# Performance work log

Measured on AMD Instinct MI355X. Metric: run time of the kernel, lower is better.

The kernel has to match this reference:

```python
import jax, jax.numpy as jnp
import numpy as np

D_MODEL = 2048
N_HEADS = 32
N_KV = 8
N_REP = N_HEADS // N_KV  # 4
HEAD_DIM = D_MODEL // N_HEADS  # 64
ROPE_BASE = 10000.0
B, T = 2, 2048


def rope_tables(seq_len, head_dim):
    inv_freq = 1.0 / (ROPE_BASE ** (jnp.arange(0, head_dim, 2, dtype=jnp.float32) / head_dim))
    t = jnp.arange(seq_len, dtype=jnp.float32)
    freqs = jnp.outer(t, inv_freq)            # [T, hd/2]
    emb = jnp.concatenate([freqs, freqs], -1)  # [T, hd]
    return jnp.cos(emb), jnp.sin(emb)


def rotate_half(x):
    x1, x2 = jnp.split(x, 2, axis=-1)
    return jnp.concatenate([-x2, x1], axis=-1)


def setup_inputs() -> dict:
    key = jax.random.key(0)
    ks = jax.random.split(key, 5)
    s = D_MODEL ** -0.5
    return {
        "x": jax.random.normal(ks[0], (B, T, D_MODEL), jnp.float32),
        "Wq": jax.random.normal(ks[1], (D_MODEL, D_MODEL), jnp.float32) * s,
        "Wk": jax.random.normal(ks[2], (D_MODEL, N_KV * HEAD_DIM), jnp.float32) * s,
        "Wv": jax.random.normal(ks[3], (D_MODEL, N_KV * HEAD_DIM), jnp.float32) * s,
        "Wo": jax.random.normal(ks[4], (D_MODEL, D_MODEL), jnp.float32) * s,
    }


def reference(x, Wq, Wk, Wv, Wo):
    Bx, Tx, C = x.shape
    # QKV projections -> [B, H, T, hd]
    q = (x @ Wq).reshape(Bx, Tx, N_HEADS, HEAD_DIM).transpose(0, 2, 1, 3)
    k = (x @ Wk).reshape(Bx, Tx, N_KV, HEAD_DIM).transpose(0, 2, 1, 3)
    v = (x @ Wv).reshape(Bx, Tx, N_KV, HEAD_DIM).transpose(0, 2, 1, 3)
    # RoPE (offset=0, no cache -> prefill path)
    cos, sin = rope_tables(Tx, HEAD_DIM)  # [T, hd]
    cos = cos[None, None]
    sin = sin[None, None]
    q = q * cos + rotate_half(q) * sin
    k = k * cos + rotate_half(k) * sin
    # Grouped causal attention without materializing expanded KV:
    # q grouped as [B, n_kv, n_rep, T, hd] shares each kv head across n_rep q heads.
    scale = HEAD_DIM ** -0.5
    qg = q.reshape(Bx, N_KV, N_REP, Tx, HEAD_DIM)
    scores = jnp.einsum('bgrtd,bgsd->bgrts', qg, k) * scale  # [B, g, r, T, S]
    causal = jnp.tril(jnp.ones((Tx, Tx), dtype=bool))
    scores = jnp.where(causal, scores, jnp.float32(-jnp.inf))
    attn = jax.nn.softmax(scores, axis=-1)
    out = jnp.einsum('bgrts,bgsd->bgrtd', attn, v)  # [B, g, r, T, hd]
    out = out.reshape(Bx, N_HEADS, Tx, HEAD_DIM).transpose(0, 2, 1, 3).reshape(Bx, Tx, C)
    return out @ Wo, k, v
```

## Files before the change

kernel.cpp:

```cpp
#include <hip/hip_runtime.h>
#include <hip/hip_bf16.h>
#include <cstdint>

typedef uint16_t u16;
typedef __attribute__((ext_vector_type(8))) __bf16 bf16x8;
typedef __attribute__((ext_vector_type(4))) float f32x4;
typedef __attribute__((ext_vector_type(16))) float f32x16;
typedef __attribute__((ext_vector_type(8))) unsigned short u16x8;

#define GLD_LDS(SRC, DST) \
  __builtin_amdgcn_global_load_lds((const __attribute__((address_space(1))) void*)(SRC), \
                                   (__attribute__((address_space(3))) void*)(DST), 16, 0, 0)

#define PSWAP(d, s) asm volatile("v_permlane32_swap_b32 %0, %1" : "+v"(d), "+v"(s))

__device__ __forceinline__ u16 f2bf(float f) {
  uint32_t u = __float_as_uint(f);
  u += 0x7fffu + ((u >> 16) & 1u);
  return (u16)(u >> 16);
}

__device__ __forceinline__ float bf2f(u16 u) {
  return __uint_as_float(((uint32_t)u) << 16);
}

__device__ __forceinline__ uint32_t pk2(float a, float b) {
  union { __bf16 h[2]; uint32_t u; } x;
  x.h[0] = (__bf16)a; x.h[1] = (__bf16)b;
  return x.u;
}

__device__ __forceinline__ float fexp2(float x) {
#if __has_builtin(__builtin_amdgcn_exp2f)
  return __builtin_amdgcn_exp2f(x);
#else
  return exp2f(x);
#endif
}

__global__ __launch_bounds__(256) void prep_all(const float* __restrict__ x, u16* __restrict__ Xb,
    const float* __restrict__ Wq, const float* __restrict__ Wk, const float* __restrict__ Wv,
    u16* __restrict__ Wcat, float* __restrict__ cosT, float* __restrict__ sinT) {
  int bid = blockIdx.x, tid = threadIdx.x;
  if (bid < 2048) {
    int base = bid * 1024 + tid;
    #pragma unroll
    for (int k = 0; k < 4; ++k) {
      int i = base + k * 256;
      float4 v = reinterpret_cast<const float4*>(x)[i];
      ushort4 o;
      o.x = f2bf(v.x); o.y = f2bf(v.y); o.z = f2bf(v.z); o.w = f2bf(v.w);
      reinterpret_cast<ushort4*>(Xb)[i] = o;
    }
    return;
  }
  if (bid >= 8192) {
    int b2 = bid - 8192;
    int t = b2 * 8 + (tid >> 5), i = tid & 31;
    float invf = powf(10000.0f, -(float)i * (1.0f / 32.0f));
    float ang = (float)t * invf;
    cosT[t * 32 + i] = cosf(ang);
    sinT[t * 32 + i] = sinf(ang);
    return;
  }
  __shared__ float tile[32][33];
  const float* W; u16* Wt; int N, bx, by;
  if (bid < 6144)      { int b2 = bid - 2048; W = Wq; Wt = Wcat;               N = 2048; bx = b2 & 63; by = b2 >> 6; }
  else if (bid < 7168) { int b2 = bid - 6144; W = Wk; Wt = Wcat + 2048 * 2048; N = 512;  bx = b2 & 15; by = b2 >> 4; }
  else                 { int b2 = bid - 7168; W = Wv; Wt = Wcat + 2560 * 2048; N = 512;  bx = b2 & 15; by = b2 >> 4; }
  int n0 = bx * 32, k0 = by * 32;
  int tx = tid & 31, ty = tid >> 5;
  #pragma unroll
  for (int i = ty; i < 32; i += 8)
    tile[i][tx] = W[(size_t)(k0 + i) * N + n0 + tx];
  __syncthreads();
  #pragma unroll
  for (int i = ty; i < 32; i += 8)
    Wt[(size_t)(n0 + i) * 2048 + k0 + tx] = f2bf(tile[tx][i]);
}

__global__ __launch_bounds__(512, 2) void gemm_qkv_wot(const u16* __restrict__ A,
    const u16* __restrict__ Bt, const float* __restrict__ Wo,
    u16* __restrict__ Cq, u16* __restrict__ WoT) {
  __shared__ alignas(16) u16 Asm[2][2][256][32];
  __shared__ alignas(16) u16 Bsm[2][2][256][32];

  const int bid = blockIdx.x;
  const int tid = threadIdx.x;

  if (bid >= 192) {
    float (*tile)[65] = (float(*)[65])&Asm[0][0][0][0];
    int b2 = bid - 192;
    int r = tid >> 3, c0 = (tid & 7) * 8;
    for (int it = 0; it < 16; ++it) {
      int tI = b2 + (it << 6);
      int k0 = (tI >> 5) * 64;
      int n0 = (tI & 31) * 64;
      if (it) __syncthreads();
      float4 v0 = *reinterpret_cast<const float4*>(&Wo[(size_t)(k0 + r) * 2048 + n0 + c0]);
      float4 v1 = *reinterpret_cast<const float4*>(&Wo[(size_t)(k0 + r) * 2048 + n0 + c0 + 4]);
      tile[r][c0 + 0] = v0.x; tile[r][c0 + 1] = v0.y; tile[r][c0 + 2] = v0.z; tile[r][c0 + 3] = v0.w;
      tile[r][c0 + 4] = v1.x; tile[r][c0 + 5] = v1.y; tile[r][c0 + 6] = v1.z; tile[r][c0 + 7] = v1.w;
      __syncthreads();
      u16x8 o;
      #pragma unroll
      for (int j = 0; j < 8; ++j) o[j] = f2bf(tile[c0 + j][r]);
      *reinterpret_cast<u16x8*>(&WoT[(size_t)(n0 + r) * 2048 + k0 + c0]) = o;
    }
    return;
  }

  const int K = 2048, N = 3072;
  const int l = tid & 63;
  const int w = tid >> 6;
  const int wm = w >> 2, wn = w & 3;
  const int l15 = l & 15, l4 = l >> 4;
  const int m0 = (bid / 12) * 256, n0 = (bid % 12) * 256;
  const int NT = K >> 6;

  f32x4 acc[8][4] = {};

  const int srow = tid >> 2;
  const int sg   = (tid & 3) ^ ((srow >> 1) & 3);
  const u16* Ag = A + (size_t)(m0 + srow) * K + sg * 8;
  const u16* Bg = Bt + (size_t)(n0 + srow) * K + sg * 8;
  const size_t rsk = (size_t)128 * K;
  char* AsD = (char*)&Asm[0][0][0][0] + tid * 16;
  char* BsD = (char*)&Bsm[0][0][0][0] + tid * 16;

#define STAGE_A(BUF, KH, KT) do { \
    GLD_LDS(Ag + (KT) + (KH) * 32,       AsD + ((BUF) * 2 + (KH)) * 16384); \
    GLD_LDS(Ag + (KT) + (KH) * 32 + rsk, AsD + ((BUF) * 2 + (KH)) * 16384 + 8192); \
  } while (0)
#define STAGE_B(BUF, KH, KT) do { \
    GLD_LDS(Bg + (KT) + (KH) * 32,       BsD + ((BUF) * 2 + (KH)) * 16384); \
    GLD_LDS(Bg + (KT) + (KH) * 32 + rsk, BsD + ((BUF) * 2 + (KH)) * 16384 + 8192); \
  } while (0)

  STAGE_A(0, 0, 0);  STAGE_B(0, 0, 0);
  STAGE_A(0, 1, 0);  STAGE_B(0, 1, 0);
  STAGE_A(1, 0, 64); STAGE_B(1, 0, 64);

  const int swz = (l15 >> 1) & 3;

  for (int t = 0; t < NT; ++t) {
    const int c = t & 1;
    const int ktn  = (t + 1) << 6;
    const int ktn2 = (t + 2) << 6;
    bf16x8 bfv[4], af[4];

    if (t < NT - 1) { asm volatile("s_waitcnt vmcnt(8)" ::: "memory"); }
    else            { asm volatile("s_waitcnt vmcnt(4)" ::: "memory"); }
    asm volatile("s_barrier" ::: "memory");
    #pragma unroll
    for (int mf = 0; mf < 4; ++mf)
      af[mf] = *(const bf16x8*)&Asm[c][0][wm * 128 + mf * 16 + l15][(l4 ^ swz) * 8];
    #pragma unroll
    for (int nf = 0; nf < 4; ++nf)
      bfv[nf] = *(const bf16x8*)&Bsm[c][0][wn * 64 + nf * 16 + l15][(l4 ^ swz) * 8];
    if (t + 1 < NT) STAGE_A(c ^ 1, 1, ktn);
    __builtin_amdgcn_s_setprio(1);
    #pragma unroll
    for (int mf = 0; mf < 4; ++mf)
      #pragma unroll
      for (int nf = 0; nf < 4; ++nf)
        acc[mf][nf] = __builtin_amdgcn_mfma_f32_16x16x32_bf16(af[mf], bfv[nf], acc[mf][nf], 0, 0, 0);
    __builtin_amdgcn_s_setprio(0);
    asm volatile("s_barrier" ::: "memory");

    #pragma unroll
    for (int mf = 0; mf < 4; ++mf)
      af[mf] = *(const bf16x8*)&Asm[c][0][wm * 128 + 64 + mf * 16 + l15][(l4 ^ swz) * 8];
    if (t + 1 < NT) STAGE_B(c ^ 1, 1, ktn);
    __builtin_amdgcn_s_setprio(1);
    #pragma unroll
    for (int mf = 0; mf < 4; ++mf)
      #pragma unroll
      for (int nf = 0; nf < 4; ++nf)
        acc[4 + mf][nf] = __builtin_amdgcn_mfma_f32_16x16x32_bf16(af[mf], bfv[nf], acc[4 + mf][nf], 0, 0, 0);
    __builtin_amdgcn_s_setprio(0);
    asm volatile("s_barrier" ::: "memory");

    if (t < NT - 1) { asm volatile("s_waitcnt vmcnt(8)" ::: "memory"); }
    else            { asm volatile("s_waitcnt vmcnt(0)" ::: "memory"); }
    asm volatile("s_barrier" ::: "memory");
    #pragma unroll
    for (int mf = 0; mf < 4; ++mf)
      af[mf] = *(const bf16x8*)&Asm[c][1][wm * 128 + mf * 16 + l15][(l4 ^ swz) * 8];
    #pragma unroll
    for (int nf = 0; nf < 4; ++nf)
      bfv[nf] = *(const bf16x8*)&Bsm[c][1][wn * 64 + nf * 16 + l15][(l4 ^ swz) * 8];
    if (t + 2 < NT) STAGE_A(c, 0, ktn2);
    __builtin_amdgcn_s_setprio(1);
    #pragma unroll
    for (int mf = 0; mf < 4; ++mf)
      #pragma unroll
      for (int nf = 0; nf < 4; ++nf)
        acc[mf][nf] = __builtin_amdgcn_mfma_f32_16x16x32_bf16(af[mf], bfv[nf], acc[mf][nf], 0, 0, 0);
    __builtin_amdgcn_s_setprio(0);
    asm volatile("s_barrier" ::: "memory");

    #pragma unroll
    for (int mf = 0; mf < 4; ++mf)
      af[mf] = *(const bf16x8*)&Asm[c][1][wm * 128 + 64 + mf * 16 + l15][(l4 ^ swz) * 8];
    if (t + 2 < NT) STAGE_B(c, 0, ktn2);
    __builtin_amdgcn_s_setprio(1);
    #pragma unroll
    for (int mf = 0; mf < 4; ++mf)
      #pragma unroll
      for (int nf = 0; nf < 4; ++nf)
        acc[4 + mf][nf] = __builtin_amdgcn_mfma_f32_16x16x32_bf16(af[mf], bfv[nf], acc[4 + mf][nf], 0, 0, 0);
    __builtin_amdgcn_s_setprio(0);
    asm volatile("s_barrier" ::: "memory");
  }
#undef STAGE_A
#undef STAGE_B

  #pragma unroll
  for (int mi = 0; mi < 8; ++mi)
    #pragma unroll
    for (int nf = 0; nf < 4; ++nf)
      #pragma unroll
      for (int r = 0; r < 4; ++r) {
        int row = m0 + wm * 128 + mi * 16 + l4 * 4 + r;
        int col = n0 + wn * 64 + nf * 16 + l15;
        Cq[(size_t)row * N + col] = f2bf(acc[mi][nf][r]);
      }
}

__global__ __launch_bounds__(512, 2) void gemm128(const u16* __restrict__ A,
    const u16* __restrict__ Bt, float* __restrict__ C, int M, int N, int K) {
  __shared__ alignas(16) u16 Asm[2][2][128][32];
  __shared__ alignas(16) u16 Bsm[2][2][256][32];

  const int tid = threadIdx.x;
  const int l = tid & 63;
  const int w = tid >> 6;
  const int wm = w >> 2, wn = w & 3;
  const int l15 = l & 15, l4 = l >> 4;
  const int m0 = blockIdx.y * 128, n0 = blockIdx.x * 256;
  const int NT = K >> 6;

  f32x4 acc[4][4] = {};

  const int srow = tid >> 2;
  const int sg   = (tid & 3) ^ ((srow >> 1) & 3);
  const u16* Ag = A + (size_t)(m0 + srow) * K + sg * 8;
  const u16* Bg = Bt + (size_t)(n0 + srow) * K + sg * 8;
  const size_t rsk = (size_t)128 * K;
  char* AsD = (char*)&Asm[0][0][0][0] + tid * 16;
  char* BsD = (char*)&Bsm[0][0][0][0] + tid * 16;

#define STG(BUF, KH, KT) do { \
    GLD_LDS(Ag + (KT) + (KH) * 32,       AsD + ((BUF) * 2 + (KH)) * 8192); \
    GLD_LDS(Bg + (KT) + (KH) * 32,       BsD + ((BUF) * 2 + (KH)) * 16384); \
    GLD_LDS(Bg + (KT) + (KH) * 32 + rsk, BsD + ((BUF) * 2 + (KH)) * 16384 + 8192); \
  } while (0)

  STG(0, 0, 0); STG(0, 1, 0); STG(1, 0, 64);

  const int swz = (l15 >> 1) & 3;

  for (int t = 0; t < NT; ++t) {
    const int c = t & 1;
    bf16x8 af[4], bfv[4];

    if (t < NT - 1) { asm volatile("s_waitcnt vmcnt(6)" ::: "memory"); }
    else            { asm volatile("s_waitcnt vmcnt(3)" ::: "memory"); }
    asm volatile("s_barrier" ::: "memory");
    #pragma unroll
    for (int mf = 0; mf < 4; ++mf)
      af[mf] = *(const bf16x8*)&Asm[c][0][wm * 64 + mf * 16 + l15][(l4 ^ swz) * 8];
    #pragma unroll
    for (int nf = 0; nf < 4; ++nf)
      bfv[nf] = *(const bf16x8*)&Bsm[c][0][wn * 64 + nf * 16 + l15][(l4 ^ swz) * 8];
    if (t + 1 < NT) STG(c ^ 1, 1, (t + 1) << 6);
    __builtin_amdgcn_s_setprio(1);
    #pragma unroll
    for (int mf = 0; mf < 4; ++mf)
      #pragma unroll
      for (int nf = 0; nf < 4; ++nf)
        acc[mf][nf] = __builtin_amdgcn_mfma_f32_16x16x32_bf16(af[mf], bfv[nf], acc[mf][nf], 0, 0, 0);
    __builtin_amdgcn_s_setprio(0);
    asm volatile("s_barrier" ::: "memory");

    if (t < NT - 1) { asm volatile("s_waitcnt vmcnt(6)" ::: "memory"); }
    else            { asm volatile("s_waitcnt vmcnt(0)" ::: "memory"); }
    asm volatile("s_barrier" ::: "memory");
    #pragma unroll
    for (int mf = 0; mf < 4; ++mf)
      af[mf] = *(const bf16x8*)&Asm[c][1][wm * 64 + mf * 16 + l15][(l4 ^ swz) * 8];
    #pragma unroll
    for (int nf = 0; nf < 4; ++nf)
      bfv[nf] = *(const bf16x8*)&Bsm[c][1][wn * 64 + nf * 16 + l15][(l4 ^ swz) * 8];
    if (t + 2 < NT) STG(c, 0, (t + 2) << 6);
    __builtin_amdgcn_s_setprio(1);
    #pragma unroll
    for (int mf = 0; mf < 4; ++mf)
      #pragma unroll
      for (int nf = 0; nf < 4; ++nf)
        acc[mf][nf] = __builtin_amdgcn_mfma_f32_16x16x32_bf16(af[mf], bfv[nf], acc[mf][nf], 0, 0, 0);
    __builtin_amdgcn_s_setprio(0);
    asm volatile("s_barrier" ::: "memory");
  }
#undef STG

  #pragma unroll
  for (int mf = 0; mf < 4; ++mf)
    #pragma unroll
    for (int nf = 0; nf < 4; ++nf)
      #pragma unroll
      for (int r = 0; r < 4; ++r) {
        int row = m0 + wm * 64 + mf * 16 + l4 * 4 + r;
        int col = n0 + wn * 64 + nf * 16 + l15;
        C[(size_t)row * N + col] = acc[mf][nf][r];
      }
}

__global__ __launch_bounds__(256) void rope_scatter(const u16* __restrict__ QKV,
    const float* __restrict__ cosT, const float* __restrict__ sinT,
    u16* __restrict__ Qr, u16* __restrict__ Kr,
    float* __restrict__ outK, float* __restrict__ outV) {
  const float QSCALE = 0.125f * 1.44269504088896f;
  int row = blockIdx.x;
  int b = row >> 11, t = row & 2047;
  const u16* src = QKV + (size_t)row * 3072;
  int tid = threadIdx.x;
  #pragma unroll
  for (int p = tid; p < 1024; p += 256) {
    int h = p >> 5, d = p & 31;
    float c = cosT[t * 32 + d], s = sinT[t * 32 + d];
    float q0 = bf2f(src[h * 64 + d]), q1 = bf2f(src[h * 64 + d + 32]);
    size_t base = ((size_t)(b * 32 + h) * 2048 + t) * 64 + d;
    Qr[base]      = f2bf((q0 * c - q1 * s) * QSCALE);
    Qr[base + 32] = f2bf((q1 * c + q0 * s) * QSCALE);
  }
  {
    int p = tid;
    int gk = p >> 5, d = p & 31;
    float c = cosT[t * 32 + d], s = sinT[t * 32 + d];
    float k0 = bf2f(src[2048 + gk * 64 + d]), k1 = bf2f(src[2048 + gk * 64 + d + 32]);
    float r0 = k0 * c - k1 * s, r1 = k1 * c + k0 * s;
    size_t base = ((size_t)(b * 8 + gk) * 2048 + t) * 64 + d;
    Kr[base] = f2bf(r0); Kr[base + 32] = f2bf(r1);
    outK[base] = r0; outK[base + 32] = r1;
  }
  #pragma unroll
  for (int p = tid; p < 512; p += 256) {
    int gv = p >> 6, d = p & 63;
    size_t base = ((size_t)(b * 8 + gv) * 2048 + t) * 64 + d;
    outV[base] = bf2f(src[2560 + gv * 64 + d]);
  }
}

__global__ __launch_bounds__(256) void v_transpose(const float* __restrict__ src, u16* __restrict__ dst) {
  __shared__ float tile[64][65];
  int tt = blockIdx.x, bg = blockIdx.y;
  int tid = threadIdx.x;
  const float* sp = src + (size_t)bg * 2048 * 64 + (size_t)tt * 64 * 64;
  int tl = tid >> 2, c0 = (tid & 3) * 16;
  #pragma unroll
  for (int i = 0; i < 4; ++i) {
    float4 v = *reinterpret_cast<const float4*>(sp + (size_t)tl * 64 + c0 + i * 4);
    tile[tl][c0 + i * 4 + 0] = v.x;
    tile[tl][c0 + i * 4 + 1] = v.y;
    tile[tl][c0 + i * 4 + 2] = v.z;
    tile[tl][c0 + i * 4 + 3] = v.w;
  }
  __syncthreads();
  int d = tid >> 2, j0 = (tid & 3) * 16;
  u16x8 a, c;
  #pragma unroll
  for (int j = 0; j < 8; ++j) a[j] = f2bf(tile[j0 + j][d]);
  #pragma unroll
  for (int j = 0; j < 8; ++j) c[j] = f2bf(tile[j0 + 8 + j][d]);
  u16* dp = dst + (size_t)bg * 64 * 2048 + (size_t)d * 2048 + tt * 64 + j0;
  *reinterpret_cast<u16x8*>(dp) = a;
  *reinterpret_cast<u16x8*>(dp + 8) = c;
}

__global__ __launch_bounds__(256) void attn_kernel(
    const u16* __restrict__ Qr, const u16* __restrict__ Kr,
    const u16* __restrict__ Vt, u16* __restrict__ Ao) {
  __shared__ alignas(16) u16 Ks[2][64][72];
  __shared__ alignas(16) u16 Vs[2][64][72];

  const float FIXEDM = 24.0f;

  int bid = blockIdx.x;
  int pairI = bid >> 5;
  int sub = (bid >> 4) & 1;
  int g   = (bid >> 1) & 7;
  int b   = bid & 1;
  int tid = threadIdx.x;
  int w = tid >> 6, l = tid & 63;
  int l31 = l & 31, hi = l >> 5;
  int h = g * 4 + w;

  const u16* Kh = Kr + (size_t)(b * 8 + g) * 2048 * 64;
  const u16* Vh = Vt + (size_t)(b * 8 + g) * 64 * 2048;

  union { u16x8 u; bf16x8 v; } ones;
  #pragma unroll
  for (int i = 0; i < 8; ++i) ones.u[i] = 0x3F80;

  int srow = tid >> 2, sc0 = (tid & 3) * 16;
  const u16* Kp = Kh + (size_t)srow * 64 + sc0;
  const u16* Vp = Vh + (size_t)srow * 2048 + sc0;

  for (int half = 0; half < 2; ++half) {
    const int qc  = half ? pairI : (31 - pairI);
    const int q0w = qc * 64 + sub * 32;
    const int qg  = q0w + l31;

    const u16* Qh = Qr + ((size_t)(b * 32 + h) * 2048 + q0w) * 64;
    bf16x8 qf[4];
    #pragma unroll
    for (int t = 0; t < 4; ++t)
      qf[t] = *reinterpret_cast<const bf16x8*>(Qh + (size_t)l31 * 64 + t * 16 + hi * 8);

    f32x16 o0 = {}, o1 = {}, lacc = {};

    if (half) __syncthreads();

    {
      bf16x8 k0v = *reinterpret_cast<const bf16x8*>(Kp);
      bf16x8 k1v = *reinterpret_cast<const bf16x8*>(Kp + 8);
      bf16x8 v0v = *reinterpret_cast<const bf16x8*>(Vp);
      bf16x8 v1v = *reinterpret_cast<const bf16x8*>(Vp + 8);
      *reinterpret_cast<bf16x8*>(&Ks[0][srow][sc0]) = k0v;
      *reinterpret_cast<bf16x8*>(&Ks[0][srow][sc0 + 8]) = k1v;
      *reinterpret_cast<bf16x8*>(&Vs[0][srow][sc0]) = v0v;
      *reinterpret_cast<bf16x8*>(&Vs[0][srow][sc0 + 8]) = v1v;
    }
    __syncthreads();

    for (int s = 0; s <= qc; ++s) {
      int cur = s & 1;
      bf16x8 knx0, knx1, vnx0, vnx1;
      if (s < qc) {
        knx0 = *reinterpret_cast<const bf16x8*>(Kp + (size_t)(s + 1) * 4096);
        knx1 = *reinterpret_cast<const bf16x8*>(Kp + (size_t)(s + 1) * 4096 + 8);
        vnx0 = *reinterpret_cast<const bf16x8*>(Vp + (size_t)(s + 1) * 64);
        vnx1 = *reinterpret_cast<const bf16x8*>(Vp + (size_t)(s + 1) * 64 + 8);
      }
      int nh = (s == qc && sub == 0) ? 1 : 2;

      f32x16 s0, s1;
      #pragma unroll
      for (int r = 0; r < 16; ++r) { s0[r] = -FIXEDM; s1[r] = -FIXEDM; }

      __builtin_amdgcn_s_setprio(1);
      #pragma unroll
      for (int t = 0; t < 4; ++t) {
        bf16x8 kf0 = *reinterpret_cast<const bf16x8*>(&Ks[cur][l31][t * 16 + hi * 8]);
        s0 = __builtin_amdgcn_mfma_f32_32x32x16_bf16(kf0, qf[t], s0, 0, 0, 0);
      }
      if (nh == 2) {
        #pragma unroll
        for (int t = 0; t < 4; ++t) {
          bf16x8 kf1 = *reinterpret_cast<const bf16x8*>(&Ks[cur][32 + l31][t * 16 + hi * 8]);
          s1 = __builtin_amdgcn_mfma_f32_32x32x16_bf16(kf1, qf[t], s1, 0, 0, 0);
        }
      }
      __builtin_amdgcn_s_setprio(0);

      if (s == qc) {
        #pragma unroll
        for (int r = 0; r < 16; ++r) {
          int kvg = s * 64 + (r & 3) + (r >> 2) * 8 + hi * 4;
          if (kvg > qg) s0[r] = -INFINITY;
        }
        if (nh == 2) {
          #pragma unroll
          for (int r = 0; r < 16; ++r) {
            int kvg = s * 64 + 32 + (r & 3) + (r >> 2) * 8 + hi * 4;
            if (kvg > qg) s1[r] = -INFINITY;
          }
        }
      }

      float p0[16], p1[16];
      #pragma unroll
      for (int r = 0; r < 16; ++r) p0[r] = fexp2(s0[r]);
      if (nh == 2) {
        #pragma unroll
        for (int r = 0; r < 16; ++r) p1[r] = fexp2(s1[r]);
      }

      uint32_t pkA[8], pkB[8];
      #pragma unroll
      for (int gi = 0; gi < 8; ++gi) {
        if (gi < nh * 4) {
          const float* pp = (gi < 4) ? p0 : p1;
          int base = (gi & 3) * 4;
          pkA[gi] = pk2(pp[base + 0], pp[base + 1]);
          pkB[gi] = pk2(pp[base + 2], pp[base + 3]);
        }
      }
      __builtin_amdgcn_s_setprio(1);
      #pragma unroll
      for (int kc = 0; kc < 4; ++kc) {
        if (kc < nh * 2) {
          uint32_t wd0 = pkA[kc * 2], wd2 = pkA[kc * 2 + 1];
          PSWAP(wd0, wd2);
          uint32_t wd1 = pkB[kc * 2], wd3 = pkB[kc * 2 + 1];
          PSWAP(wd1, wd3);
          union { uint32_t wd[4]; bf16x8 v; } pb;
          pb.wd[0] = wd0; pb.wd[1] = wd1; pb.wd[2] = wd2; pb.wd[3] = wd3;
          bf16x8 va0 = *reinterpret_cast<const bf16x8*>(&Vs[cur][l31][kc * 16 + hi * 8]);
          bf16x8 va1 = *reinterpret_cast<const bf16x8*>(&Vs[cur][32 + l31][kc * 16 + hi * 8]);
          o0 = __builtin_amdgcn_mfma_f32_32x32x16_bf16(va0, pb.v, o0, 0, 0, 0);
          o1 = __builtin_amdgcn_mfma_f32_32x32x16_bf16(va1, pb.v, o1, 0, 0, 0);
          lacc = __builtin_amdgcn_mfma_f32_32x32x16_bf16(ones.v, pb.v, lacc, 0, 0, 0);
        }
      }
      __builtin_amdgcn_s_setprio(0);

      if (s < qc) {
        *reinterpret_cast<bf16x8*>(&Ks[cur ^ 1][srow][sc0]) = knx0;
        *reinterpret_cast<bf16x8*>(&Ks[cur ^ 1][srow][sc0 + 8]) = knx1;
        *reinterpret_cast<bf16x8*>(&Vs[cur ^ 1][srow][sc0]) = vnx0;
        *reinterpret_cast<bf16x8*>(&Vs[cur ^ 1][srow][sc0 + 8]) = vnx1;
        __syncthreads();
      }
    }

    float inv = 1.0f / lacc[0];
    int token = b * 2048 + q0w + l31;
    u16* dst = Ao + (size_t)token * 2048 + h * 64;
    #pragma unroll
    for (int hf = 0; hf < 2; ++hf) {
      f32x16 ov = hf ? o1 : o0;
      #pragma unroll
      for (int r = 0; r < 16; r += 2) {
        int d = (r & 3) + (r >> 2) * 8 + hi * 4 + hf * 32;
        *reinterpret_cast<uint32_t*>(dst + d) = pk2(ov[r] * inv, ov[r + 1] * inv);
      }
    }
  }
}

extern "C" void kernel_launch(void* const* d_in, const int* in_sizes, int n_in,
                              void* d_out, int out_size, void* d_ws, size_t ws_size,
                              hipStream_t stream) {
  const float* x  = (const float*)d_in[0];
  const float* Wq = (const float*)d_in[1];
  const float* Wk = (const float*)d_in[2];
  const float* Wv = (const float*)d_in[3];
  const float* Wo = (const float*)d_in[4];
  float* out = (float*)d_out;

  char* ws = (char*)d_ws;
  u16*   Xb    = (u16*)(ws + 0);
  u16*   Wcat  = (u16*)(ws + 16777216);
  u16*   WoT   = (u16*)(ws + 29360128);
  u16*   QKV   = (u16*)(ws + 37748736);
  u16*   AttnB = (u16*)(ws + 37748736);
  u16*   Qr    = (u16*)(ws + 88080384);
  u16*   Kr    = (u16*)(ws + 104857600);
  u16*   Vtr   = (u16*)(ws + 109051904);
  float* cosT  = (float*)(ws + 113246208);
  float* sinT  = (float*)(ws + 113508352);

  float* outK = out + 8388608;
  float* outV = out + 10485760;

  prep_all<<<8448, 256, 0, stream>>>(x, Xb, Wq, Wk, Wv, Wcat, cosT, sinT);
  gemm_qkv_wot<<<256, 512, 0, stream>>>(Xb, Wcat, Wo, QKV, WoT);
  rope_scatter<<<4096, 256, 0, stream>>>(QKV, cosT, sinT, Qr, Kr, outK, outV);
  v_transpose<<<dim3(32, 16), 256, 0, stream>>>(outV, Vtr);
  attn_kernel<<<512, 256, 0, stream>>>(Qr, Kr, Vtr, AttnB);
  gemm128<<<dim3(8, 32), 512, 0, stream>>>(AttnB, WoT, out, 4096, 2048, 2048);
}
```

Before: 202.7 us.

## Move Wo transpose into prep kernel and retile QKV GEMM to 128x384

The Wo fp32-to-bf16 transpose moves out of the QKV GEMM kernel and into the prep kernel as extra 32x32 tile blocks. The QKV GEMM is retiled from 256x256 blocks with a 2x4 warp grid to 128x384 blocks, each warp owning a 128x48 strip, launched as an 8x32 grid of 256 blocks. The aim is to spread the GEMM evenly across CUs without the transpose blocks sharing its launch, and to simplify the staging schedule. In exchange, A-fragment reuse per warp drops, and the launch bound no longer requests two blocks per CU.

Result: slower. 210.8 us (+4.0%).

```diff
diff --git a/kernel.cpp b/kernel.cpp
--- a/kernel.cpp
+++ b/kernel.cpp
@@ -40,7 +40,8 @@
 
 __global__ __launch_bounds__(256) void prep_all(const float* __restrict__ x, u16* __restrict__ Xb,
     const float* __restrict__ Wq, const float* __restrict__ Wk, const float* __restrict__ Wv,
-    u16* __restrict__ Wcat, float* __restrict__ cosT, float* __restrict__ sinT) {
+    const float* __restrict__ Wo, u16* __restrict__ Wcat, u16* __restrict__ WoT,
+    float* __restrict__ cosT, float* __restrict__ sinT) {
   int bid = blockIdx.x, tid = threadIdx.x;
   if (bid < 2048) {
     int base = bid * 1024 + tid;
@@ -54,7 +55,7 @@
     }
     return;
   }
-  if (bid >= 8192) {
+  if (bid >= 8192 && bid < 8448) {
     int b2 = bid - 8192;
     int t = b2 * 8 + (tid >> 5), i = tid & 31;
     float invf = powf(10000.0f, -(float)i * (1.0f / 32.0f));
@@ -67,7 +68,8 @@
   const float* W; u16* Wt; int N, bx, by;
   if (bid < 6144)      { int b2 = bid - 2048; W = Wq; Wt = Wcat;               N = 2048; bx = b2 & 63; by = b2 >> 6; }
   else if (bid < 7168) { int b2 = bid - 6144; W = Wk; Wt = Wcat + 2048 * 2048; N = 512;  bx = b2 & 15; by = b2 >> 4; }
-  else                 { int b2 = bid - 7168; W = Wv; Wt = Wcat + 2560 * 2048; N = 512;  bx = b2 & 15; by = b2 >> 4; }
+  else if (bid < 8192) { int b2 = bid - 7168; W = Wv; Wt = Wcat + 2560 * 2048; N = 512;  bx = b2 & 15; by = b2 >> 4; }
+  else                 { int b2 = bid - 8448; W = Wo; Wt = WoT;                N = 2048; bx = b2 & 63; by = b2 >> 6; }
   int n0 = bx * 32, k0 = by * 32;
   int tx = tid & 31, ty = tid >> 5;
   #pragma unroll
@@ -79,46 +81,20 @@
     Wt[(size_t)(n0 + i) * 2048 + k0 + tx] = f2bf(tile[tx][i]);
 }
 
-__global__ __launch_bounds__(512, 2) void gemm_qkv_wot(const u16* __restrict__ A,
-    const u16* __restrict__ Bt, const float* __restrict__ Wo,
-    u16* __restrict__ Cq, u16* __restrict__ WoT) {
-  __shared__ alignas(16) u16 Asm[2][2][256][32];
-  __shared__ alignas(16) u16 Bsm[2][2][256][32];
-
-  const int bid = blockIdx.x;
+__global__ __launch_bounds__(512) void gemm_qkv(const u16* __restrict__ A,
+    const u16* __restrict__ Bt, u16* __restrict__ Cq) {
+  __shared__ alignas(16) u16 Asm[2][2][128][32];
+  __shared__ alignas(16) u16 Bsm[2][2][384][32];
+
+  const int K = 2048, N = 3072;
   const int tid = threadIdx.x;
-
-  if (bid >= 192) {
-    float (*tile)[65] = (float(*)[65])&Asm[0][0][0][0];
-    int b2 = bid - 192;
-    int r = tid >> 3, c0 = (tid & 7) * 8;
-    for (int it = 0; it < 16; ++it) {
-      int tI = b2 + (it << 6);
-      int k0 = (tI >> 5) * 64;
-      int n0 = (tI & 31) * 64;
-      if (it) __syncthreads();
-      float4 v0 = *reinterpret_cast<const float4*>(&Wo[(size_t)(k0 + r) * 2048 + n0 + c0]);
-      float4 v1 = *reinterpret_cast<const float4*>(&Wo[(size_t)(k0 + r) * 2048 + n0 + c0 + 4]);
-      tile[r][c0 + 0] = v0.x; tile[r][c0 + 1] = v0.y; tile[r][c0 + 2] = v0.z; tile[r][c0 + 3] = v0.w;
-      tile[r][c0 + 4] = v1.x; tile[r][c0 + 5] = v1.y; tile[r][c0 + 6] = v1.z; tile[r][c0 + 7] = v1.w;
-      __syncthreads();
-      u16x8 o;
-      #pragma unroll
-      for (int j = 0; j < 8; ++j) o[j] = f2bf(tile[c0 + j][r]);
-      *reinterpret_cast<u16x8*>(&WoT[(size_t)(n0 + r) * 2048 + k0 + c0]) = o;
-    }
-    return;
-  }
-
-  const int K = 2048, N = 3072;
   const int l = tid & 63;
   const int w = tid >> 6;
-  const int wm = w >> 2, wn = w & 3;
   const int l15 = l & 15, l4 = l >> 4;
-  const int m0 = (bid / 12) * 256, n0 = (bid % 12) * 256;
+  const int m0 = blockIdx.y * 128, n0 = blockIdx.x * 384;
   const int NT = K >> 6;
 
-  f32x4 acc[8][4] = {};
+  f32x4 acc[8][3] = {};
 
   const int srow = tid >> 2;
   const int sg   = (tid & 3) ^ ((srow >> 1) & 3);
@@ -128,56 +104,37 @@
   char* AsD = (char*)&Asm[0][0][0][0] + tid * 16;
   char* BsD = (char*)&Bsm[0][0][0][0] + tid * 16;
 
-#define STAGE_A(BUF, KH, KT) do { \
-    GLD_LDS(Ag + (KT) + (KH) * 32,       AsD + ((BUF) * 2 + (KH)) * 16384); \
-    GLD_LDS(Ag + (KT) + (KH) * 32 + rsk, AsD + ((BUF) * 2 + (KH)) * 16384 + 8192); \
+#define STG(BUF, KH, KT) do { \
+    GLD_LDS(Ag + (KT) + (KH) * 32,           AsD + ((BUF) * 2 + (KH)) * 8192); \
+    GLD_LDS(Bg + (KT) + (KH) * 32,           BsD + ((BUF) * 2 + (KH)) * 24576); \
+    GLD_LDS(Bg + (KT) + (KH) * 32 + rsk,     BsD + ((BUF) * 2 + (KH)) * 24576 + 8192); \
+    GLD_LDS(Bg + (KT) + (KH) * 32 + 2 * rsk, BsD + ((BUF) * 2 + (KH)) * 24576 + 16384); \
   } while (0)
-#define STAGE_B(BUF, KH, KT) do { \
-    GLD_LDS(Bg + (KT) + (KH) * 32,       BsD + ((BUF) * 2 + (KH)) * 16384); \
-    GLD_LDS(Bg + (KT) + (KH) * 32 + rsk, BsD + ((BUF) * 2 + (KH)) * 16384 + 8192); \
-  } while (0)
-
-  STAGE_A(0, 0, 0);  STAGE_B(0, 0, 0);
-  STAGE_A(0, 1, 0);  STAGE_B(0, 1, 0);
-  STAGE_A(1, 0, 64); STAGE_B(1, 0, 64);
+
+  STG(0, 0, 0); STG(0, 1, 0); STG(1, 0, 64);
 
   const int swz = (l15 >> 1) & 3;
+  const int c0w = w * 48;
 
   for (int t = 0; t < NT; ++t) {
     const int c = t & 1;
-    const int ktn  = (t + 1) << 6;
-    const int ktn2 = (t + 2) << 6;
-    bf16x8 bfv[4], af[4];
+    bf16x8 bfv[3];
 
     if (t < NT - 1) { asm volatile("s_waitcnt vmcnt(8)" ::: "memory"); }
     else            { asm volatile("s_waitcnt vmcnt(4)" ::: "memory"); }
     asm volatile("s_barrier" ::: "memory");
     #pragma unroll
-    for (int mf = 0; mf < 4; ++mf)
-      af[mf] = *(const bf16x8*)&Asm[c][0][wm * 128 + mf * 16 + l15][(l4 ^ swz) * 8];
-    #pragma unroll
-    for (int nf = 0; nf < 4; ++nf)
-      bfv[nf] = *(const bf16x8*)&Bsm[c][0][wn * 64 + nf * 16 + l15][(l4 ^ swz) * 8];
-    if (t + 1 < NT) STAGE_A(c ^ 1, 1, ktn);
+    for (int nf = 0; nf < 3; ++nf)
+      bfv[nf] = *(const bf16x8*)&Bsm[c][0][c0w + nf * 16 + l15][(l4 ^ swz) * 8];
+    if (t + 1 < NT) STG(c ^ 1, 1, (t + 1) << 6);
     __builtin_amdgcn_s_setprio(1);
     #pragma unroll
-    for (int mf = 0; mf < 4; ++mf)
-      #pragma unroll
-      for (int nf = 0; nf < 4; ++nf)
-        acc[mf][nf] = __builtin_amdgcn_mfma_f32_16x16x32_bf16(af[mf], bfv[nf], acc[mf][nf], 0, 0, 0);
-    __builtin_amdgcn_s_setprio(0);
-    asm volatile("s_barrier" ::: "memory");
-
-    #pragma unroll
-    for (int mf = 0; mf < 4; ++mf)
-      af[mf] = *(const bf16x8*)&Asm[c][0][wm * 128 + 64 + mf * 16 + l15][(l4 ^ swz) * 8];
-    if (t + 1 < NT) STAGE_B(c ^ 1, 1, ktn);
-    __builtin_amdgcn_s_setprio(1);
-    #pragma unroll
-    for (int mf = 0; mf < 4; ++mf)
-      #pragma unroll
-      for (int nf = 0; nf < 4; ++nf)
-        acc[4 + mf][nf] = __builtin_amdgcn_mfma_f32_16x16x32_bf16(af[mf], bfv[nf], acc[4 + mf][nf], 0, 0, 0);
+    for (int mf = 0; mf < 8; ++mf) {
+      bf16x8 af = *(const bf16x8*)&Asm[c][0][mf * 16 + l15][(l4 ^ swz) * 8];
+      #pragma unroll
+      for (int nf = 0; nf < 3; ++nf)
+        acc[mf][nf] = __builtin_amdgcn_mfma_f32_16x16x32_bf16(af, bfv[nf], acc[mf][nf], 0, 0, 0);
+    }
     __builtin_amdgcn_s_setprio(0);
     asm volatile("s_barrier" ::: "memory");
 
@@ -185,46 +142,31 @@
     else            { asm volatile("s_waitcnt vmcnt(0)" ::: "memory"); }
     asm volatile("s_barrier" ::: "memory");
     #pragma unroll
-    for (int mf = 0; mf < 4; ++mf)
-      af[mf] = *(const bf16x8*)&Asm[c][1][wm * 128 + mf * 16 + l15][(l4 ^ swz) * 8];
-    #pragma unroll
-    for (int nf = 0; nf < 4; ++nf)
-      bfv[nf] = *(const bf16x8*)&Bsm[c][1][wn * 64 + nf * 16 + l15][(l4 ^ swz) * 8];
-    if (t + 2 < NT) STAGE_A(c, 0, ktn2);
+    for (int nf = 0; nf < 3; ++nf)
+      bfv[nf] = *(const bf16x8*)&Bsm[c][1][c0w + nf * 16 + l15][(l4 ^ swz) * 8];
+    if (t + 2 < NT) STG(c, 0, (t + 2) << 6);
     __builtin_amdgcn_s_setprio(1);
     #pragma unroll
-    for (int mf = 0; mf < 4; ++mf)
-      #pragma unroll
-      for (int nf = 0; nf < 4; ++nf)
-        acc[mf][nf] = __builtin_amdgcn_mfma_f32_16x16x32_bf16(af[mf], bfv[nf], acc[mf][nf], 0, 0, 0);
+    for (int mf = 0; mf < 8; ++mf) {
+      bf16x8 af = *(const bf16x8*)&Asm[c][1][mf * 16 + l15][(l4 ^ swz) * 8];
+      #pragma unroll
+      for (int nf = 0; nf < 3; ++nf)
+        acc[mf][nf] = __builtin_amdgcn_mfma_f32_16x16x32_bf16(af, bfv[nf], acc[mf][nf], 0, 0, 0);
+    }
     __builtin_amdgcn_s_setprio(0);
     asm volatile("s_barrier" ::: "memory");
-
-    #pragma unroll
-    for (int mf = 0; mf < 4; ++mf)
-      af[mf] = *(const bf16x8*)&Asm[c][1][wm * 128 + 64 + mf * 16 + l15][(l4 ^ swz) * 8];
-    if (t + 2 < NT) STAGE_B(c, 0, ktn2);
-    __builtin_amdgcn_s_setprio(1);
-    #pragma unroll
-    for (int mf = 0; mf < 4; ++mf)
-      #pragma unroll
-      for (int nf = 0; nf < 4; ++nf)
-        acc[4 + mf][nf] = __builtin_amdgcn_mfma_f32_16x16x32_bf16(af[mf], bfv[nf], acc[4 + mf][nf], 0, 0, 0);
-    __builtin_amdgcn_s_setprio(0);
-    asm volatile("s_barrier" ::: "memory");
-  }
-#undef STAGE_A
-#undef STAGE_B
-
-  #pragma unroll
-  for (int mi = 0; mi < 8; ++mi)
-    #pragma unroll
-    for (int nf = 0; nf < 4; ++nf)
+  }
+#undef STG
+
+  #pragma unroll
+  for (int mf = 0; mf < 8; ++mf)
+    #pragma unroll
+    for (int nf = 0; nf < 3; ++nf)
       #pragma unroll
       for (int r = 0; r < 4; ++r) {
-        int row = m0 + wm * 128 + mi * 16 + l4 * 4 + r;
-        int col = n0 + wn * 64 + nf * 16 + l15;
-        Cq[(size_t)row * N + col] = f2bf(acc[mi][nf][r]);
+        int row = m0 + mf * 16 + l4 * 4 + r;
+        int col = n0 + c0w + nf * 16 + l15;
+        Cq[(size_t)row * N + col] = f2bf(acc[mf][nf][r]);
       }
 }
 
@@ -566,8 +508,8 @@
   float* outK = out + 8388608;
   float* outV = out + 10485760;
 
-  prep_all<<<8448, 256, 0, stream>>>(x, Xb, Wq, Wk, Wv, Wcat, cosT, sinT);
-  gemm_qkv_wot<<<256, 512, 0, stream>>>(Xb, Wcat, Wo, QKV, WoT);
+  prep_all<<<12544, 256, 0, stream>>>(x, Xb, Wq, Wk, Wv, Wo, Wcat, WoT, cosT, sinT);
+  gemm_qkv<<<dim3(8, 32), 512, 0, stream>>>(Xb, Wcat, QKV);
   rope_scatter<<<4096, 256, 0, stream>>>(QKV, cosT, sinT, Qr, Kr, outK, outV);
   v_transpose<<<dim3(32, 16), 256, 0, stream>>>(outV, Vtr);
   attn_kernel<<<512, 256, 0, stream>>>(Qr, Kr, Vtr, AttnB);
```

## Move Wo transpose into prep kernel and prefetch A fragments before MFMA halves

Applied to the files above, without the earlier changes.

The Wo fp32→bf16 transpose moves out of the extra blocks of the QKV GEMM and into the prep_all kernel as 4096 additional 32x32 tile blocks, so the GEMM launches only its 192 compute tiles on a 2D grid. Inside the GEMM main loop, both halves of the A fragments are now loaded from LDS up front, and one of the per-k-half barriers is removed. This should shorten the GEMM's tail and reduce synchronisation. The cost is more live registers (af0/af1) and a longer prep kernel.

Measured after the change: 195.3 us, median of 2. -3.6%, faster.

```diff
diff --git a/kernel.cpp b/kernel.cpp
--- a/kernel.cpp
+++ b/kernel.cpp
@@ -40,7 +40,8 @@
 
 __global__ __launch_bounds__(256) void prep_all(const float* __restrict__ x, u16* __restrict__ Xb,
     const float* __restrict__ Wq, const float* __restrict__ Wk, const float* __restrict__ Wv,
-    u16* __restrict__ Wcat, float* __restrict__ cosT, float* __restrict__ sinT) {
+    const float* __restrict__ Wo, u16* __restrict__ Wcat, u16* __restrict__ WoT,
+    float* __restrict__ cosT, float* __restrict__ sinT) {
   int bid = blockIdx.x, tid = threadIdx.x;
   if (bid < 2048) {
     int base = bid * 1024 + tid;
@@ -54,7 +55,7 @@
     }
     return;
   }
-  if (bid >= 8192) {
+  if (bid >= 8192 && bid < 8448) {
     int b2 = bid - 8192;
     int t = b2 * 8 + (tid >> 5), i = tid & 31;
     float invf = powf(10000.0f, -(float)i * (1.0f / 32.0f));
@@ -67,7 +68,8 @@
   const float* W; u16* Wt; int N, bx, by;
   if (bid < 6144)      { int b2 = bid - 2048; W = Wq; Wt = Wcat;               N = 2048; bx = b2 & 63; by = b2 >> 6; }
   else if (bid < 7168) { int b2 = bid - 6144; W = Wk; Wt = Wcat + 2048 * 2048; N = 512;  bx = b2 & 15; by = b2 >> 4; }
-  else                 { int b2 = bid - 7168; W = Wv; Wt = Wcat + 2560 * 2048; N = 512;  bx = b2 & 15; by = b2 >> 4; }
+  else if (bid < 8192) { int b2 = bid - 7168; W = Wv; Wt = Wcat + 2560 * 2048; N = 512;  bx = b2 & 15; by = b2 >> 4; }
+  else                 { int b2 = bid - 8448; W = Wo; Wt = WoT;                N = 2048; bx = b2 & 63; by = b2 >> 6; }
   int n0 = bx * 32, k0 = by * 32;
   int tx = tid & 31, ty = tid >> 5;
   #pragma unroll
@@ -79,43 +81,18 @@
     Wt[(size_t)(n0 + i) * 2048 + k0 + tx] = f2bf(tile[tx][i]);
 }
 
-__global__ __launch_bounds__(512, 2) void gemm_qkv_wot(const u16* __restrict__ A,
-    const u16* __restrict__ Bt, const float* __restrict__ Wo,
-    u16* __restrict__ Cq, u16* __restrict__ WoT) {
+__global__ __launch_bounds__(512, 2) void gemm_qkv(const u16* __restrict__ A,
+    const u16* __restrict__ Bt, u16* __restrict__ Cq) {
   __shared__ alignas(16) u16 Asm[2][2][256][32];
   __shared__ alignas(16) u16 Bsm[2][2][256][32];
 
-  const int bid = blockIdx.x;
+  const int K = 2048, N = 3072;
   const int tid = threadIdx.x;
-
-  if (bid >= 192) {
-    float (*tile)[65] = (float(*)[65])&Asm[0][0][0][0];
-    int b2 = bid - 192;
-    int r = tid >> 3, c0 = (tid & 7) * 8;
-    for (int it = 0; it < 16; ++it) {
-      int tI = b2 + (it << 6);
-      int k0 = (tI >> 5) * 64;
-      int n0 = (tI & 31) * 64;
-      if (it) __syncthreads();
-      float4 v0 = *reinterpret_cast<const float4*>(&Wo[(size_t)(k0 + r) * 2048 + n0 + c0]);
-      float4 v1 = *reinterpret_cast<const float4*>(&Wo[(size_t)(k0 + r) * 2048 + n0 + c0 + 4]);
-      tile[r][c0 + 0] = v0.x; tile[r][c0 + 1] = v0.y; tile[r][c0 + 2] = v0.z; tile[r][c0 + 3] = v0.w;
-      tile[r][c0 + 4] = v1.x; tile[r][c0 + 5] = v1.y; tile[r][c0 + 6] = v1.z; tile[r][c0 + 7] = v1.w;
-      __syncthreads();
-      u16x8 o;
-      #pragma unroll
-      for (int j = 0; j < 8; ++j) o[j] = f2bf(tile[c0 + j][r]);
-      *reinterpret_cast<u16x8*>(&WoT[(size_t)(n0 + r) * 2048 + k0 + c0]) = o;
-    }
-    return;
-  }
-
-  const int K = 2048, N = 3072;
   const int l = tid & 63;
   const int w = tid >> 6;
   const int wm = w >> 2, wn = w & 3;
   const int l15 = l & 15, l4 = l >> 4;
-  const int m0 = (bid / 12) * 256, n0 = (bid % 12) * 256;
+  const int m0 = blockIdx.y * 256, n0 = blockIdx.x * 256;
   const int NT = K >> 6;
 
   f32x4 acc[8][4] = {};
@@ -147,37 +124,35 @@
     const int c = t & 1;
     const int ktn  = (t + 1) << 6;
     const int ktn2 = (t + 2) << 6;
-    bf16x8 bfv[4], af[4];
+    bf16x8 bfv[4], af0[4], af1[4];
 
     if (t < NT - 1) { asm volatile("s_waitcnt vmcnt(8)" ::: "memory"); }
     else            { asm volatile("s_waitcnt vmcnt(4)" ::: "memory"); }
     asm volatile("s_barrier" ::: "memory");
     #pragma unroll
-    for (int mf = 0; mf < 4; ++mf)
-      af[mf] = *(const bf16x8*)&Asm[c][0][wm * 128 + mf * 16 + l15][(l4 ^ swz) * 8];
-    #pragma unroll
     for (int nf = 0; nf < 4; ++nf)
       bfv[nf] = *(const bf16x8*)&Bsm[c][0][wn * 64 + nf * 16 + l15][(l4 ^ swz) * 8];
+    #pragma unroll
+    for (int mf = 0; mf < 4; ++mf)
+      af0[mf] = *(const bf16x8*)&Asm[c][0][wm * 128 + mf * 16 + l15][(l4 ^ swz) * 8];
     if (t + 1 < NT) STAGE_A(c ^ 1, 1, ktn);
+    #pragma unroll
+    for (int mf = 0; mf < 4; ++mf)
+      af1[mf] = *(const bf16x8*)&Asm[c][0][wm * 128 + 64 + mf * 16 + l15][(l4 ^ swz) * 8];
     __builtin_amdgcn_s_setprio(1);
     #pragma unroll
     for (int mf = 0; mf < 4; ++mf)
       #pragma unroll
       for (int nf = 0; nf < 4; ++nf)
-        acc[mf][nf] = __builtin_amdgcn_mfma_f32_16x16x32_bf16(af[mf], bfv[nf], acc[mf][nf], 0, 0, 0);
+        acc[mf][nf] = __builtin_amdgcn_mfma_f32_16x16x32_bf16(af0[mf], bfv[nf], acc[mf][nf], 0, 0, 0);
     __builtin_amdgcn_s_setprio(0);
-    asm volatile("s_barrier" ::: "memory");
-
-    #pragma unroll
-    for (int mf = 0; mf < 4; ++mf)
-      af[mf] = *(const bf16x8*)&Asm[c][0][wm * 128 + 64 + mf * 16 + l15][(l4 ^ swz) * 8];
     if (t + 1 < NT) STAGE_B(c ^ 1, 1, ktn);
     __builtin_amdgcn_s_setprio(1);
     #pragma unroll
     for (int mf = 0; mf < 4; ++mf)
       #pragma unroll
       for (int nf = 0; nf < 4; ++nf)
-        acc[4 + mf][nf] = __builtin_amdgcn_mfma_f32_16x16x32_bf16(af[mf], bfv[nf], acc[4 + mf][nf], 0, 0, 0);
+        acc[4 + mf][nf] = __builtin_amdgcn_mfma_f32_16x16x32_bf16(af1[mf], bfv[nf], acc[4 + mf][nf], 0, 0, 0);
     __builtin_amdgcn_s_setprio(0);
     asm volatile("s_barrier" ::: "memory");
 
@@ -185,31 +160,29 @@
     else            { asm volatile("s_waitcnt vmcnt(0)" ::: "memory"); }
     asm volatile("s_barrier" ::: "memory");
     #pragma unroll
-    for (int mf = 0; mf < 4; ++mf)
-      af[mf] = *(const bf16x8*)&Asm[c][1][wm * 128 + mf * 16 + l15][(l4 ^ swz) * 8];
-    #pragma unroll
     for (int nf = 0; nf < 4; ++nf)
       bfv[nf] = *(const bf16x8*)&Bsm[c][1][wn * 64 + nf * 16 + l15][(l4 ^ swz) * 8];
+    #pragma unroll
+    for (int mf = 0; mf < 4; ++mf)
+      af0[mf] = *(const bf16x8*)&Asm[c][1][wm * 128 + mf * 16 + l15][(l4 ^ swz) * 8];
     if (t + 2 < NT) STAGE_A(c, 0, ktn2);
+    #pragma unroll
+    for (int mf = 0; mf < 4; ++mf)
+      af1[mf] = *(const bf16x8*)&Asm[c][1][wm * 128 + 64 + mf * 16 + l15][(l4 ^ swz) * 8];
     __builtin_amdgcn_s_setprio(1);
     #pragma unroll
     for (int mf = 0; mf < 4; ++mf)
       #pragma unroll
       for (int nf = 0; nf < 4; ++nf)
-        acc[mf][nf] = __builtin_amdgcn_mfma_f32_16x16x32_bf16(af[mf], bfv[nf], acc[mf][nf], 0, 0, 0);
+        acc[mf][nf] = __builtin_amdgcn_mfma_f32_16x16x32_bf16(af0[mf], bfv[nf], acc[mf][nf], 0, 0, 0);
     __builtin_amdgcn_s_setprio(0);
-    asm volatile("s_barrier" ::: "memory");
-
-    #pragma unroll
-    for (int mf = 0; mf < 4; ++mf)
-      af[mf] = *(const bf16x8*)&Asm[c][1][wm * 128 + 64 + mf * 16 + l15][(l4 ^ swz) * 8];
     if (t + 2 < NT) STAGE_B(c, 0, ktn2);
     __builtin_amdgcn_s_setprio(1);
     #pragma unroll
     for (int mf = 0; mf < 4; ++mf)
       #pragma unroll
       for (int nf = 0; nf < 4; ++nf)
-        acc[4 + mf][nf] = __builtin_amdgcn_mfma_f32_16x16x32_bf16(af[mf], bfv[nf], acc[4 + mf][nf], 0, 0, 0);
+        acc[4 + mf][nf] = __builtin_amdgcn_mfma_f32_16x16x32_bf16(af1[mf], bfv[nf], acc[4 + mf][nf], 0, 0, 0);
     __builtin_amdgcn_s_setprio(0);
     asm volatile("s_barrier" ::: "memory");
   }
@@ -566,8 +539,8 @@
   float* outK = out + 8388608;
   float* outV = out + 10485760;
 
-  prep_all<<<8448, 256, 0, stream>>>(x, Xb, Wq, Wk, Wv, Wcat, cosT, sinT);
-  gemm_qkv_wot<<<256, 512, 0, stream>>>(Xb, Wcat, Wo, QKV, WoT);
+  prep_all<<<12544, 256, 0, stream>>>(x, Xb, Wq, Wk, Wv, Wo, Wcat, WoT, cosT, sinT);
+  gemm_qkv<<<dim3(12, 16), 512, 0, stream>>>(Xb, Wcat, QKV);
   rope_scatter<<<4096, 256, 0, stream>>>(QKV, cosT, sinT, Qr, Kr, outK, outV);
   v_transpose<<<dim3(32, 16), 256, 0, stream>>>(outV, Vtr);
   attn_kernel<<<512, 256, 0, stream>>>(Qr, Kr, Vtr, AttnB);
```
